# Performance work log

Hardware: AMD Instinct MI355X
Metric: run time of the kernel (lower is better)

The kernel has to match this reference:

```python
import jax, jax.numpy as jnp
import numpy as np

B = 16384      # number of batched 6-node FC graphs
A = 6          # num_agents (nodes per graph)
D_OBS = 128    # raw observation dim
D_EMB = 250    # embedding / GAT feature dim
H = 3          # GAT heads (head outputs averaged to keep dim 250)
HID = 256
N_ACT = 5
NEG_SLOPE = 0.2


def setup_inputs() -> dict:
    key = jax.random.key(0)
    ks = jax.random.split(key, 16)
    def w(i, shape, scale=0.05):
        return jax.random.normal(ks[i], shape, dtype=jnp.float32) * scale
    return {
        "x": jax.random.normal(ks[0], (B * A, D_OBS), dtype=jnp.float32),
        "W_emb": w(1, (D_OBS, D_EMB)), "b_emb": jnp.zeros((D_EMB,), jnp.float32),
        "W_gat": w(2, (H, D_EMB, D_EMB)),
        "a_l": w(3, (H, D_EMB)), "a_r": w(4, (H, D_EMB)),
        "W1": w(5, (2 * D_EMB, HID)), "b1": jnp.zeros((HID,), jnp.float32),
        "W2": w(6, (HID, N_ACT)), "b2": jnp.zeros((N_ACT,), jnp.float32),
        "V1": w(7, (2 * D_EMB, HID)), "vb1": jnp.zeros((HID,), jnp.float32),
        "V2": w(8, (HID, 1)), "vb2": jnp.zeros((1,), jnp.float32),
    }


def reference(x, W_emb, b_emb, W_gat, a_l, a_r, W1, b1, W2, b2, V1, vb1, V2, vb2):
    # embedding layer
    h = jax.nn.relu(x @ W_emb + b_emb)                       # [N, 250]
    hb = h.reshape(B, A, D_EMB)                              # [B, 6, 250]
    # GAT on fully-connected 6-node graphs (incl. self edges), dense-masked form
    Wh = jnp.einsum("bad,hde->bhae", hb, W_gat)              # [B, H, 6, 250]
    el = jnp.einsum("bhae,he->bha", Wh, a_l)                 # dst term
    er = jnp.einsum("bhae,he->bha", Wh, a_r)                 # src term
    e = jax.nn.leaky_relu(el[:, :, :, None] + er[:, :, None, :], NEG_SLOPE)  # [B,H,6,6]
    attn = jax.nn.softmax(e, axis=-1)                        # edge softmax over neighbors
    gat = jnp.einsum("bhij,bhje->bhie", attn, Wh).mean(axis=1)  # mean over heads -> [B,6,250]
    feat = jnp.concatenate([hb, gat], axis=-1).reshape(B * A, 2 * D_EMB)  # [N, 500]
    # actor head (reg1)
    probs = jax.nn.softmax(jax.nn.relu(feat @ W1 + b1) @ W2 + b2, axis=-1)  # [N, 5]
    # critic head (reg2)
    value = jax.nn.relu(feat @ V1 + vb1) @ V2 + vb2           # [N, 1]
    return jnp.concatenate([probs, value], axis=-1)          # [N, 6]
```

## Files before the change

kernel.cpp:

```cpp
#include <hip/hip_runtime.h>

typedef unsigned short u16;
typedef unsigned int   u32;
typedef unsigned long long u64;
typedef __attribute__((ext_vector_type(4))) int   i32x4;
typedef __attribute__((ext_vector_type(4))) float f32x4;
typedef __attribute__((ext_vector_type(8))) short s16x8;

#define NROWS 98304L
#define LDF   512

__device__ __forceinline__ u16 f2bf(float x) {
  union { float f; u32 u; } v; v.f = x;
  return (u16)((v.u + 0x7FFFu + ((v.u >> 16) & 1u)) >> 16);
}
__device__ __forceinline__ float bf2f(u16 b) {
  union { float f; u32 u; } v; v.u = ((u32)b) << 16;
  return v.f;
}

__global__ __launch_bounds__(256)
void prep_weights(const float* __restrict__ W_emb, const float* __restrict__ b_emb,
                  const float* __restrict__ W_gat, const float* __restrict__ W1,
                  const float* __restrict__ b1, const float* __restrict__ V1,
                  const float* __restrict__ vb1,
                  u16* __restrict__ Wemb_t, u16* __restrict__ Wgat_t,
                  u16* __restrict__ W1V1_t, float* __restrict__ bembp,
                  float* __restrict__ b1vb1)
{
  const int idx = blockIdx.x * 256 + threadIdx.x;
  const int stride = gridDim.x * 256;
  for (int t = idx; t < 256 * 128; t += stride) {
    int n = t >> 7, k = t & 127;
    Wemb_t[t] = f2bf(n < 250 ? W_emb[k * 250 + n] : 0.f);
  }
  for (int t = idx; t < 3 * 256 * 256; t += stride) {
    int h = t >> 16, rem = t & 65535, e = rem >> 8, d = rem & 255;
    Wgat_t[t] = f2bf((e < 250 && d < 250) ? W_gat[(h * 250 + d) * 250 + e] : 0.f);
  }
  for (int t = idx; t < 512 * 512; t += stride) {
    int n = t >> 9, k = t & 511;
    const float* src = (n < 256) ? W1 : V1;
    int col = n & 255;
    float v = 0.f;
    if (k < 250) v = src[k * 256 + col];
    else if (k >= 256 && k < 506) v = src[(k - 6) * 256 + col];
    W1V1_t[t] = f2bf(v);
  }
  for (int t = idx; t < 512; t += stride) b1vb1[t] = (t < 256) ? b1[t] : vb1[t - 256];
  for (int t = idx; t < 256; t += stride) bembp[t] = (t < 250) ? b_emb[t] : 0.f;
}

__global__ __launch_bounds__(256)
void cvt_x(const float* __restrict__ x, u16* __restrict__ xb)
{
  const long n = NROWS * 128;
  long i = ((long)blockIdx.x * 256 + threadIdx.x) * 8;
  const long stride = (long)gridDim.x * 256 * 8;
  for (; i < n; i += stride) {
    f32x4 a = *(const f32x4*)(x + i);
    f32x4 b = *(const f32x4*)(x + i + 4);
    i32x4 o;
    o[0] = (int)((u32)f2bf(a[0]) | ((u32)f2bf(a[1]) << 16));
    o[1] = (int)((u32)f2bf(a[2]) | ((u32)f2bf(a[3]) << 16));
    o[2] = (int)((u32)f2bf(b[0]) | ((u32)f2bf(b[1]) << 16));
    o[3] = (int)((u32)f2bf(b[2]) | ((u32)f2bf(b[3]) << 16));
    *(i32x4*)(xb + i) = o;
  }
}

template<int KSTEPS, int EPI>
__global__ __launch_bounds__(256, 2)
void gemm_bf16(const u16* __restrict__ A, int lda,
               const u16* __restrict__ B, int ldb, long strideB,
               u16* __restrict__ C, int ldc, long strideC,
               const float* __restrict__ bias)
{
  __shared__ __align__(16) u16 At[128][72];
  __shared__ __align__(16) u16 Bt[128][72];
  const int tid = threadIdx.x;
  const int w = tid >> 6, lane = tid & 63;
  const int fl = lane & 15, fh = lane >> 4;
  const int wr = (w >> 1) * 64, wc = (w & 1) * 64;
  const int srow = tid >> 3, soff = (tid & 7) * 8;

  const u16* Ab = A + (long)blockIdx.x * 128 * lda;
  const u16* Bb = B + (long)blockIdx.z * strideB + (long)blockIdx.y * 128 * ldb;
  u16* Cb = C + (long)blockIdx.z * strideC + (long)blockIdx.x * 128 * ldc + blockIdx.y * 128;
  const float* biasb = bias + blockIdx.y * 128;

  f32x4 acc[4][4];
  #pragma unroll
  for (int m = 0; m < 4; m++)
    #pragma unroll
    for (int n = 0; n < 4; n++)
      acc[m][n] = f32x4{0.f, 0.f, 0.f, 0.f};

  i32x4 av[4], bv[4];
  #pragma unroll
  for (int i = 0; i < 4; i++) {
    av[i] = *(const i32x4*)(Ab + (long)(i * 32 + srow) * lda + soff);
    bv[i] = *(const i32x4*)(Bb + (long)(i * 32 + srow) * ldb + soff);
  }
  for (int ks = 0;;) {
    __syncthreads();
    #pragma unroll
    for (int i = 0; i < 4; i++) {
      *(i32x4*)(&At[i * 32 + srow][soff]) = av[i];
      *(i32x4*)(&Bt[i * 32 + srow][soff]) = bv[i];
    }
    __syncthreads();
    ++ks;
    if (ks < KSTEPS) {
      #pragma unroll
      for (int i = 0; i < 4; i++) {
        av[i] = *(const i32x4*)(Ab + (long)(i * 32 + srow) * lda + ks * 64 + soff);
        bv[i] = *(const i32x4*)(Bb + (long)(i * 32 + srow) * ldb + ks * 64 + soff);
      }
    }
    #pragma unroll
    for (int kk = 0; kk < 2; kk++) {
      s16x8 af[4], bf[4];
      #pragma unroll
      for (int m = 0; m < 4; m++) af[m] = *(const s16x8*)(&At[wr + m * 16 + fl][kk * 32 + fh * 8]);
      #pragma unroll
      for (int n = 0; n < 4; n++) bf[n] = *(const s16x8*)(&Bt[wc + n * 16 + fl][kk * 32 + fh * 8]);
      #pragma unroll
      for (int m = 0; m < 4; m++)
        #pragma unroll
        for (int n = 0; n < 4; n++)
          acc[m][n] = __builtin_amdgcn_mfma_f32_16x16x32_bf16(af[m], bf[n], acc[m][n], 0, 0, 0);
    }
    if (ks >= KSTEPS) break;
  }
  #pragma unroll
  for (int m = 0; m < 4; m++) {
    const int r0 = wr + m * 16 + fh * 4;
    #pragma unroll
    for (int n = 0; n < 4; n++) {
      const int col = wc + n * 16 + fl;
      float bvv = 0.f;
      if constexpr (EPI == 1) bvv = biasb[col];
      f32x4 v = acc[m][n];
      #pragma unroll
      for (int r = 0; r < 4; r++) {
        float xv = v[r];
        if constexpr (EPI == 1) xv = fmaxf(xv + bvv, 0.f);
        Cb[(long)(r0 + r) * ldc + col] = f2bf(xv);
      }
    }
  }
}

__global__ __launch_bounds__(256)
void attn_gat(const u16* __restrict__ Wh, const float* __restrict__ a_l,
              const float* __restrict__ a_r, u16* __restrict__ feat)
{
  const int w = threadIdx.x >> 6, lane = threadIdx.x & 63;
  const long g = (long)blockIdx.x * 4 + w;
  const int c0 = lane * 4;
  float gacc[6][4];
  #pragma unroll
  for (int i = 0; i < 6; i++)
    #pragma unroll
    for (int q = 0; q < 4; q++) gacc[i][q] = 0.f;

  #pragma unroll
  for (int h = 0; h < 3; h++) {
    float whf[6][4];
    #pragma unroll
    for (int i = 0; i < 6; i++) {
      u64 v = *(const u64*)(Wh + (((long)h * NROWS + g * 6 + i) << 8) + c0);
      whf[i][0] = bf2f((u16)v);
      whf[i][1] = bf2f((u16)(v >> 16));
      whf[i][2] = bf2f((u16)(v >> 32));
      whf[i][3] = bf2f((u16)(v >> 48));
    }
    float alv[4], arv[4];
    #pragma unroll
    for (int q = 0; q < 4; q++) {
      int c = c0 + q;
      alv[q] = (c < 250) ? a_l[h * 250 + c] : 0.f;
      arv[q] = (c < 250) ? a_r[h * 250 + c] : 0.f;
    }
    float pel[6], per[6];
    #pragma unroll
    for (int i = 0; i < 6; i++) {
      pel[i] = whf[i][0] * alv[0] + whf[i][1] * alv[1] + whf[i][2] * alv[2] + whf[i][3] * alv[3];
      per[i] = whf[i][0] * arv[0] + whf[i][1] * arv[1] + whf[i][2] * arv[2] + whf[i][3] * arv[3];
    }
    #pragma unroll
    for (int off = 1; off < 64; off <<= 1) {
      #pragma unroll
      for (int i = 0; i < 6; i++) {
        pel[i] += __shfl_xor(pel[i], off, 64);
        per[i] += __shfl_xor(per[i], off, 64);
      }
    }
    #pragma unroll
    for (int i = 0; i < 6; i++) {
      float e[6]; float mx = -1e30f;
      #pragma unroll
      for (int j = 0; j < 6; j++) {
        float t = pel[i] + per[j];
        t = (t > 0.f) ? t : 0.2f * t;
        e[j] = t; mx = fmaxf(mx, t);
      }
      float s = 0.f;
      #pragma unroll
      for (int j = 0; j < 6; j++) { e[j] = __expf(e[j] - mx); s += e[j]; }
      float inv = 1.f / s;
      #pragma unroll
      for (int j = 0; j < 6; j++) {
        float a = e[j] * inv;
        #pragma unroll
        for (int q = 0; q < 4; q++) gacc[i][q] += a * whf[j][q];
      }
    }
  }
  #pragma unroll
  for (int i = 0; i < 6; i++) {
    const float k = 1.f / 3.f;
    u64 o = (u64)f2bf(gacc[i][0] * k)
          | ((u64)f2bf(gacc[i][1] * k) << 16)
          | ((u64)f2bf(gacc[i][2] * k) << 32)
          | ((u64)f2bf(gacc[i][3] * k) << 48);
    *(u64*)(feat + (g * 6 + i) * LDF + 256 + c0) = o;
  }
}

__global__ __launch_bounds__(256)
void heads(const u16* __restrict__ hidden, const float* __restrict__ W2,
           const float* __restrict__ b2, const float* __restrict__ V2,
           const float* __restrict__ vb2, float* __restrict__ out)
{
  const int w = threadIdx.x >> 6, lane = threadIdx.x & 63;
  const bool actor = lane < 32;
  const int kb = (lane & 31) * 8;
  float wreg[40];
  if (actor) {
    #pragma unroll
    for (int i = 0; i < 8; i++)
      #pragma unroll
      for (int j = 0; j < 5; j++) wreg[i * 5 + j] = W2[(kb + i) * 5 + j];
  } else {
    #pragma unroll
    for (int i = 0; i < 8; i++) wreg[i] = V2[kb + i];
  }
  float b2v[5];
  #pragma unroll
  for (int j = 0; j < 5; j++) b2v[j] = b2[j];
  const float vb2v = vb2[0];

  const long base = ((long)blockIdx.x * 4 + w) * 6;
  for (int rr = 0; rr < 6; ++rr) {
    const long row = base + rr;
    const u16* hp = hidden + row * 512 + (actor ? kb : 256 + kb);
    i32x4 hv4 = *(const i32x4*)hp;
    float hv[8];
    #pragma unroll
    for (int q = 0; q < 4; q++) {
      u32 u = (u32)hv4[q];
      hv[2 * q]     = bf2f((u16)u);
      hv[2 * q + 1] = bf2f((u16)(u >> 16));
    }
    float p[6] = {0.f, 0.f, 0.f, 0.f, 0.f, 0.f};
    if (actor) {
      #pragma unroll
      for (int j = 0; j < 5; j++) {
        float s = 0.f;
        #pragma unroll
        for (int i = 0; i < 8; i++) s += hv[i] * wreg[i * 5 + j];
        p[j] = s;
      }
    } else {
      float s = 0.f;
      #pragma unroll
      for (int i = 0; i < 8; i++) s += hv[i] * wreg[i];
      p[5] = s;
    }
    #pragma unroll
    for (int off = 1; off < 64; off <<= 1)
      #pragma unroll
      for (int j = 0; j < 6; j++) p[j] += __shfl_xor(p[j], off, 64);
    if (lane < 6) {
      float val;
      if (lane < 5) {
        float lg[5]; float mx = -1e30f;
        #pragma unroll
        for (int j = 0; j < 5; j++) { lg[j] = p[j] + b2v[j]; mx = fmaxf(mx, lg[j]); }
        float s = 0.f;
        #pragma unroll
        for (int j = 0; j < 5; j++) s += __expf(lg[j] - mx);
        val = __expf(lg[lane] - mx) / s;
      } else {
        val = p[5] + vb2v;
      }
      out[row * 6 + lane] = val;
    }
  }
}

extern "C" void kernel_launch(void* const* d_in, const int* in_sizes, int n_in,
                              void* d_out, int out_size, void* d_ws, size_t ws_size,
                              hipStream_t stream)
{
  const float* x     = (const float*)d_in[0];
  const float* W_emb = (const float*)d_in[1];
  const float* b_emb = (const float*)d_in[2];
  const float* W_gat = (const float*)d_in[3];
  const float* a_l   = (const float*)d_in[4];
  const float* a_r   = (const float*)d_in[5];
  const float* W1    = (const float*)d_in[6];
  const float* b1    = (const float*)d_in[7];
  const float* W2    = (const float*)d_in[8];
  const float* b2    = (const float*)d_in[9];
  const float* V1    = (const float*)d_in[10];
  const float* vb1   = (const float*)d_in[11];
  const float* V2    = (const float*)d_in[12];
  const float* vb2   = (const float*)d_in[13];

  char* ws = (char*)d_ws;
  u16* feat = (u16*)ws;
  char* r2  = ws + 100663296L;
  u16* xb   = (u16*)r2;
  u16* Whb  = (u16*)r2;
  u16* hid  = (u16*)r2;
  char* wt  = r2 + 150994944L;
  u16*   Wemb_t = (u16*)wt;
  u16*   Wgat_t = (u16*)(wt + 65536);
  u16*   W1V1_t = (u16*)(wt + 458752);
  float* b1vb1  = (float*)(wt + 983040);
  float* bembp  = (float*)(wt + 985088);

  prep_weights<<<256, 256, 0, stream>>>(W_emb, b_emb, W_gat, W1, b1, V1, vb1,
                                        Wemb_t, Wgat_t, W1V1_t, bembp, b1vb1);
  cvt_x<<<2048, 256, 0, stream>>>(x, xb);
  gemm_bf16<2, 1><<<dim3(768, 2, 1), 256, 0, stream>>>(xb, 128, Wemb_t, 128, 0L,
                                                       feat, 512, 0L, bembp);
  gemm_bf16<4, 0><<<dim3(768, 2, 3), 256, 0, stream>>>(feat, 512, Wgat_t, 256, 65536L,
                                                       Whb, 256, 25165824L, bembp);
  attn_gat<<<4096, 256, 0, stream>>>(Whb, a_l, a_r, feat);
  gemm_bf16<8, 1><<<dim3(768, 4, 1), 256, 0, stream>>>(feat, 512, W1V1_t, 512, 0L,
                                                       hid, 512, 0L, b1vb1);
  heads<<<4096, 256, 0, stream>>>(hid, W2, b2, V2, vb2, (float*)d_out);
}
```

Baseline: 426.2 us.

## Fold attention vectors into GAT weights, use direct-to-LDS loads with swizzle

Three changes ship together. The attention projections W_gat·a_l and W_gat·a_r are precomputed as two extra padded columns of the GAT weight matrix, so the GEMM emits el/er directly and attn_gat swaps its dot products and butterfly reductions for a single lane shuffle. The GEMM now uses global_load_lds into an XOR-swizzled LDS layout in place of register staging with padded rows, but this drops the register prefetch overlap between load and compute. attn_gat also issues all Wh loads up front; the extra columns are rounded to bf16, which adds some rounding error to the attention logits.

```diff
diff --git a/kernel.cpp b/kernel.cpp
--- a/kernel.cpp
+++ b/kernel.cpp
@@ -19,9 +19,16 @@
   return v.f;
 }
 
+__device__ __forceinline__ void gload_lds16(const u16* g, u16* l) {
+  __builtin_amdgcn_global_load_lds(
+      (const __attribute__((address_space(1))) unsigned int*)g,
+      (__attribute__((address_space(3))) unsigned int*)l, 16, 0, 0);
+}
+
 __global__ __launch_bounds__(256)
 void prep_weights(const float* __restrict__ W_emb, const float* __restrict__ b_emb,
-                  const float* __restrict__ W_gat, const float* __restrict__ W1,
+                  const float* __restrict__ W_gat, const float* __restrict__ a_l,
+                  const float* __restrict__ a_r, const float* __restrict__ W1,
                   const float* __restrict__ b1, const float* __restrict__ V1,
                   const float* __restrict__ vb1,
                   u16* __restrict__ Wemb_t, u16* __restrict__ Wgat_t,
@@ -36,7 +43,17 @@
   }
   for (int t = idx; t < 3 * 256 * 256; t += stride) {
     int h = t >> 16, rem = t & 65535, e = rem >> 8, d = rem & 255;
-    Wgat_t[t] = f2bf((e < 250 && d < 250) ? W_gat[(h * 250 + d) * 250 + e] : 0.f);
+    float v = 0.f;
+    if (e < 250 && d < 250) {
+      v = W_gat[(h * 250 + d) * 250 + e];
+    } else if ((e == 250 || e == 251) && d < 250) {
+      const float* av = ((e == 250) ? a_l : a_r) + h * 250;
+      const float* wrow = W_gat + ((long)h * 250 + d) * 250;
+      float s = 0.f;
+      for (int q = 0; q < 250; q++) s += wrow[q] * av[q];
+      v = s;
+    }
+    Wgat_t[t] = f2bf(v);
   }
   for (int t = idx; t < 512 * 512; t += stride) {
     int n = t >> 9, k = t & 511;
@@ -76,13 +93,15 @@
                u16* __restrict__ C, int ldc, long strideC,
                const float* __restrict__ bias)
 {
-  __shared__ __align__(16) u16 At[128][72];
-  __shared__ __align__(16) u16 Bt[128][72];
+  __shared__ __align__(16) u16 At[128 * 64];
+  __shared__ __align__(16) u16 Bt[128 * 64];
   const int tid = threadIdx.x;
   const int w = tid >> 6, lane = tid & 63;
   const int fl = lane & 15, fh = lane >> 4;
   const int wr = (w >> 1) * 64, wc = (w & 1) * 64;
-  const int srow = tid >> 3, soff = (tid & 7) * 8;
+  const int srow = lane >> 3;
+  const int scol = (((lane & 7) ^ srow) << 3);
+  const int swz = (fl & 7) << 3;
 
   const u16* Ab = A + (long)blockIdx.x * 128 * lda;
   const u16* Bb = B + (long)blockIdx.z * strideB + (long)blockIdx.y * 128 * ldb;
@@ -96,42 +115,30 @@
     for (int n = 0; n < 4; n++)
       acc[m][n] = f32x4{0.f, 0.f, 0.f, 0.f};
 
-  i32x4 av[4], bv[4];
-  #pragma unroll
-  for (int i = 0; i < 4; i++) {
-    av[i] = *(const i32x4*)(Ab + (long)(i * 32 + srow) * lda + soff);
-    bv[i] = *(const i32x4*)(Bb + (long)(i * 32 + srow) * ldb + soff);
-  }
-  for (int ks = 0;;) {
+  for (int ks = 0; ks < KSTEPS; ks++) {
     __syncthreads();
     #pragma unroll
-    for (int i = 0; i < 4; i++) {
-      *(i32x4*)(&At[i * 32 + srow][soff]) = av[i];
-      *(i32x4*)(&Bt[i * 32 + srow][soff]) = bv[i];
+    for (int c = 0; c < 4; c++) {
+      const int row = w * 32 + c * 8 + srow;
+      gload_lds16(Ab + (long)row * lda + ks * 64 + scol, At + (w * 4 + c) * 512);
+      gload_lds16(Bb + (long)row * ldb + ks * 64 + scol, Bt + (w * 4 + c) * 512);
     }
     __syncthreads();
-    ++ks;
-    if (ks < KSTEPS) {
-      #pragma unroll
-      for (int i = 0; i < 4; i++) {
-        av[i] = *(const i32x4*)(Ab + (long)(i * 32 + srow) * lda + ks * 64 + soff);
-        bv[i] = *(const i32x4*)(Bb + (long)(i * 32 + srow) * ldb + ks * 64 + soff);
-      }
-    }
     #pragma unroll
     for (int kk = 0; kk < 2; kk++) {
-      s16x8 af[4], bf[4];
-      #pragma unroll
-      for (int m = 0; m < 4; m++) af[m] = *(const s16x8*)(&At[wr + m * 16 + fl][kk * 32 + fh * 8]);
-      #pragma unroll
-      for (int n = 0; n < 4; n++) bf[n] = *(const s16x8*)(&Bt[wc + n * 16 + fl][kk * 32 + fh * 8]);
+      s16x8 af[4], bfr[4];
       #pragma unroll
       for (int m = 0; m < 4; m++)
+        af[m] = *(const s16x8*)(At + (wr + m * 16 + fl) * 64 + ((kk * 32 + fh * 8) ^ swz));
+      #pragma unroll
+      for (int n = 0; n < 4; n++)
+        bfr[n] = *(const s16x8*)(Bt + (wc + n * 16 + fl) * 64 + ((kk * 32 + fh * 8) ^ swz));
+      #pragma unroll
+      for (int m = 0; m < 4; m++)
         #pragma unroll
         for (int n = 0; n < 4; n++)
-          acc[m][n] = __builtin_amdgcn_mfma_f32_16x16x32_bf16(af[m], bf[n], acc[m][n], 0, 0, 0);
-    }
-    if (ks >= KSTEPS) break;
+          acc[m][n] = __builtin_amdgcn_mfma_f32_16x16x32_bf16(af[m], bfr[n], acc[m][n], 0, 0, 0);
+    }
   }
   #pragma unroll
   for (int m = 0; m < 4; m++) {
@@ -153,12 +160,19 @@
 }
 
 __global__ __launch_bounds__(256)
-void attn_gat(const u16* __restrict__ Wh, const float* __restrict__ a_l,
-              const float* __restrict__ a_r, u16* __restrict__ feat)
+void attn_gat(const u16* __restrict__ Wh, u16* __restrict__ feat)
 {
   const int w = threadIdx.x >> 6, lane = threadIdx.x & 63;
   const long g = (long)blockIdx.x * 4 + w;
   const int c0 = lane * 4;
+
+  u64 raw[3][6];
+  #pragma unroll
+  for (int h = 0; h < 3; h++)
+    #pragma unroll
+    for (int i = 0; i < 6; i++)
+      raw[h][i] = *(const u64*)(Wh + (((long)h * NROWS + g * 6 + i) << 8) + c0);
+
   float gacc[6][4];
   #pragma unroll
   for (int i = 0; i < 6; i++)
@@ -170,39 +184,24 @@
     float whf[6][4];
     #pragma unroll
     for (int i = 0; i < 6; i++) {
-      u64 v = *(const u64*)(Wh + (((long)h * NROWS + g * 6 + i) << 8) + c0);
+      u64 v = raw[h][i];
       whf[i][0] = bf2f((u16)v);
       whf[i][1] = bf2f((u16)(v >> 16));
       whf[i][2] = bf2f((u16)(v >> 32));
       whf[i][3] = bf2f((u16)(v >> 48));
     }
-    float alv[4], arv[4];
-    #pragma unroll
-    for (int q = 0; q < 4; q++) {
-      int c = c0 + q;
-      alv[q] = (c < 250) ? a_l[h * 250 + c] : 0.f;
-      arv[q] = (c < 250) ? a_r[h * 250 + c] : 0.f;
-    }
-    float pel[6], per[6];
+    float el[6], er[6];
     #pragma unroll
     for (int i = 0; i < 6; i++) {
-      pel[i] = whf[i][0] * alv[0] + whf[i][1] * alv[1] + whf[i][2] * alv[2] + whf[i][3] * alv[3];
-      per[i] = whf[i][0] * arv[0] + whf[i][1] * arv[1] + whf[i][2] * arv[2] + whf[i][3] * arv[3];
-    }
-    #pragma unroll
-    for (int off = 1; off < 64; off <<= 1) {
-      #pragma unroll
-      for (int i = 0; i < 6; i++) {
-        pel[i] += __shfl_xor(pel[i], off, 64);
-        per[i] += __shfl_xor(per[i], off, 64);
-      }
+      el[i] = __shfl(whf[i][2], 62, 64);
+      er[i] = __shfl(whf[i][3], 62, 64);
     }
     #pragma unroll
     for (int i = 0; i < 6; i++) {
       float e[6]; float mx = -1e30f;
       #pragma unroll
       for (int j = 0; j < 6; j++) {
-        float t = pel[i] + per[j];
+        float t = el[i] + er[j];
         t = (t > 0.f) ? t : 0.2f * t;
         e[j] = t; mx = fmaxf(mx, t);
       }
@@ -333,14 +332,14 @@
   float* b1vb1  = (float*)(wt + 983040);
   float* bembp  = (float*)(wt + 985088);
 
-  prep_weights<<<256, 256, 0, stream>>>(W_emb, b_emb, W_gat, W1, b1, V1, vb1,
+  prep_weights<<<256, 256, 0, stream>>>(W_emb, b_emb, W_gat, a_l, a_r, W1, b1, V1, vb1,
                                         Wemb_t, Wgat_t, W1V1_t, bembp, b1vb1);
   cvt_x<<<2048, 256, 0, stream>>>(x, xb);
   gemm_bf16<2, 1><<<dim3(768, 2, 1), 256, 0, stream>>>(xb, 128, Wemb_t, 128, 0L,
                                                        feat, 512, 0L, bembp);
   gemm_bf16<4, 0><<<dim3(768, 2, 3), 256, 0, stream>>>(feat, 512, Wgat_t, 256, 65536L,
                                                        Whb, 256, 25165824L, bembp);
-  attn_gat<<<4096, 256, 0, stream>>>(Whb, a_l, a_r, feat);
+  attn_gat<<<4096, 256, 0, stream>>>(Whb, feat);
   gemm_bf16<8, 1><<<dim3(768, 4, 1), 256, 0, stream>>>(feat, 512, W1V1_t, 512, 0L,
                                                        hid, 512, 0L, b1vb1);
   heads<<<4096, 256, 0, stream>>>(hid, W2, b2, V2, vb2, (float*)d_out);
```

Measured after the change: 390.3 us. 8.4% less time.
